# Kernel optimization log

Measured on AMD Instinct MI355X. Metric: run time of the kernel, lower is better.

The kernel has to match this reference:

```python
import jax, jax.numpy as jnp
import numpy as np

B, N, F, K = 64, 4096, 128, 64
N_STEP = 4
EPS_VAR = 1e-5


def setup_inputs() -> dict:
    key = jax.random.key(0)
    k1, k2, k3 = jax.random.split(key, 3)
    emb_in = jax.random.normal(k1, (B, N, F), dtype=jnp.float32)
    # number of valid nodes per sample; must be > K so init indices are valid
    batch_nb_nodes = jax.random.randint(k2, (B,), K + 1, N + 1).astype(jnp.int32)
    mask = (jnp.arange(N)[None, :] < batch_nb_nodes[:, None]).astype(jnp.float32)
    fc_w = jax.random.normal(k3, (1, F), dtype=jnp.float32) / np.float32(np.sqrt(F))
    fc_b = jnp.zeros((1,), dtype=jnp.float32)
    init_idx = jnp.arange(K, dtype=jnp.int32)  # replaces np.random.choice
    return {"emb_in": emb_in, "mask": mask, "fc_w": fc_w, "fc_b": fc_b,
            "batch_nb_nodes": batch_nb_nodes, "init_idx": init_idx}


def spatialnorm(emb, batch_nb_nodes, mask):
    # masked per-sample, per-feature standardization over the node axis
    n = batch_nb_nodes.astype(emb.dtype)[:, None, None]        # [B,1,1]
    m = mask[:, :, None]                                       # [B,N,1]
    mean = (emb * m).sum(axis=1, keepdims=True) / n            # [B,1,F]
    var = (((emb - mean) ** 2) * m).sum(axis=1, keepdims=True) / n
    x = (emb - mean) / jnp.sqrt(var + EPS_VAR) * m
    return x, mean, var


def expectation(x, mu):
    # squared L2 dists via expansion; avoids the [B,N,K,F] diff tensor
    x2 = (x * x).sum(-1)                                       # [B,N]
    m2 = (mu * mu).sum(-1)                                     # [B,K]
    xm = jnp.einsum('bnf,bkf->bnk', x, mu)                     # [B,N,K]
    norm = x2[:, :, None] - 2.0 * xm + m2[:, None, :]
    likelihood = jnp.exp(-0.5 * norm) + 1e-20
    P = likelihood / (likelihood.sum(axis=2, keepdims=True) + 1e-40)
    return P


def maximization(x, P):
    # mu = P^T X  (note: original does NOT divide by cluster mass)
    return jnp.einsum('bnk,bnf->bkf', P, x)


def reference(emb_in, mask, fc_w, fc_b, batch_nb_nodes, init_idx):
    x, _, _ = spatialnorm(emb_in, batch_nb_nodes, mask)
    mu = x[:, init_idx]                                        # [B,K,F]
    for _ in range(N_STEP):
        P = expectation(x, mu)
        mu = maximization(x, P)
    out = jnp.einsum('bkf,of->bko', mu, fc_w) + fc_b           # fc(mu): [B,K,1]
    out = out[..., 0].mean(axis=1)                             # [B]
    return jax.nn.sigmoid(out)
```

## Files before the change

### kernel.cpp

```cpp
#include <hip/hip_runtime.h>
#include <math.h>

#define BB 64
#define NN 4096
#define FF 128
#define KK 64
#define TILE 128
#define NSTEP 4
#define SPB 32

typedef short bf16x8 __attribute__((ext_vector_type(8)));
typedef float f32x4 __attribute__((ext_vector_type(4)));

__device__ __forceinline__ ushort f2bf(float f) {
    union { float f; unsigned u; } c; c.f = f;
    unsigned r = c.u + 0x7FFFu + ((c.u >> 16) & 1u);
    return (ushort)(r >> 16);
}
__device__ __forceinline__ float bf2f(ushort h) {
    union { unsigned u; float f; } c; c.u = ((unsigned)h) << 16;
    return c.f;
}

__global__ void k_stats_part(const float* __restrict__ emb, const int* __restrict__ nbv,
                             float* __restrict__ spart) {
    int b = blockIdx.y, s = blockIdx.x;
    int nb = nbv[b];
    int t = threadIdx.x;
    int c = t & 31, rr = t >> 5;
    int n0 = s * (NN / SPB);
    int n1 = min(n0 + NN / SPB, nb);
    float4 s1 = {0,0,0,0}, s2 = {0,0,0,0};
    const float4* base = (const float4*)(emb + (size_t)b * NN * FF);
    for (int n = n0 + rr; n < n1; n += 8) {
        float4 e = base[(size_t)n * 32 + c];
        s1.x += e.x; s1.y += e.y; s1.z += e.z; s1.w += e.w;
        s2.x += e.x*e.x; s2.y += e.y*e.y; s2.z += e.z*e.z; s2.w += e.w*e.w;
    }
    __shared__ __align__(16) float4 r1[8][32];
    __shared__ __align__(16) float4 r2[8][32];
    r1[rr][c] = s1; r2[rr][c] = s2;
    __syncthreads();
    if (t < 32) {
        float4 a1 = r1[0][t], a2 = r2[0][t];
        #pragma unroll
        for (int r = 1; r < 8; ++r) {
            float4 u = r1[r][t], v = r2[r][t];
            a1.x+=u.x; a1.y+=u.y; a1.z+=u.z; a1.w+=u.w;
            a2.x+=v.x; a2.y+=v.y; a2.z+=v.z; a2.w+=v.w;
        }
        ((float4*)(spart + ((size_t)(b*SPB+s)*2 + 0)*FF))[t] = a1;
        ((float4*)(spart + ((size_t)(b*SPB+s)*2 + 1)*FF))[t] = a2;
    }
}

__global__ void k_stats_fin(const float* __restrict__ spart, const int* __restrict__ nbv,
                            float* __restrict__ meanp, float* __restrict__ rstdp) {
    int b = blockIdx.x, f = threadIdx.x;
    float s1 = 0.f, s2 = 0.f;
    for (int s = 0; s < SPB; ++s) {
        s1 += spart[((size_t)(b*SPB+s)*2 + 0)*FF + f];
        s2 += spart[((size_t)(b*SPB+s)*2 + 1)*FF + f];
    }
    float nb = (float)nbv[b];
    float mean = s1 / nb;
    float var = s2 / nb - mean * mean;
    meanp[b*FF + f] = mean;
    rstdp[b*FF + f] = rsqrtf(var + 1e-5f);
}

__global__ void k_init(const float* __restrict__ emb, const int* __restrict__ nbv,
                       const int* __restrict__ init_idx,
                       const float* __restrict__ meanp, const float* __restrict__ rstdp,
                       float* __restrict__ mu) {
    size_t i = (size_t)blockIdx.x * 256 + threadIdx.x;
    int f = (int)(i & 127);
    int k = (int)((i >> 7) & 63);
    int b = (int)(i >> 13);
    int row = init_idx[k];
    float v = 0.f;
    if (row < nbv[b]) {
        float e = emb[((size_t)b * NN + row) * FF + f];
        v = (e - meanp[b*FF + f]) * rstdp[b*FF + f];
    }
    mu[i] = v;
}

__global__ void k_split(const float* __restrict__ mu, ushort* __restrict__ muh,
                        ushort* __restrict__ mul, float* __restrict__ m2g) {
    int b = blockIdx.x, t = threadIdx.x;
    int k = t >> 2, q = t & 3;
    size_t base = ((size_t)b * KK + k) * FF + q * 32;
    float m2 = 0.f;
    #pragma unroll
    for (int it = 0; it < 8; ++it) {
        float4 v = *(const float4*)(mu + base + it*4);
        m2 += v.x*v.x + v.y*v.y + v.z*v.z + v.w*v.w;
        ushort4 h4, l4;
        h4.x = f2bf(v.x); l4.x = f2bf(v.x - bf2f(h4.x));
        h4.y = f2bf(v.y); l4.y = f2bf(v.y - bf2f(h4.y));
        h4.z = f2bf(v.z); l4.z = f2bf(v.z - bf2f(h4.z));
        h4.w = f2bf(v.w); l4.w = f2bf(v.w - bf2f(h4.w));
        *(ushort4*)(muh + base + it*4) = h4;
        *(ushort4*)(mul + base + it*4) = l4;
    }
    m2 += __shfl_xor(m2, 1); m2 += __shfl_xor(m2, 2);
    if (q == 0) m2g[b*KK + k] = m2;
}

__global__ void k_zero(float* __restrict__ p) {
    size_t i = (size_t)blockIdx.x * 256 + threadIdx.x;
    ((float4*)p)[i] = make_float4(0.f, 0.f, 0.f, 0.f);
}

__global__ __launch_bounds__(1024, 4) void k_em3(const float* __restrict__ emb,
                                                 const int* __restrict__ nbv,
                                                 const float* __restrict__ meanp,
                                                 const float* __restrict__ rstdp,
                                                 const ushort* __restrict__ muh,
                                                 const ushort* __restrict__ mul,
                                                 const float* __restrict__ m2g,
                                                 float* __restrict__ mu_out) {
    __shared__ __align__(16) ushort xTh[FF * 64];
    __shared__ __align__(16) ushort xTl[FF * 64];
    __shared__ __align__(16) ushort pTh[KK * TILE];
    __shared__ __align__(16) ushort pTl[KK * TILE];

    int bb = blockIdx.y, tt = blockIdx.x;
    int nb = nbv[bb];
    int row0 = tt * TILE;
    if (row0 >= nb) return;
    int t = threadIdx.x;
    int lane = t & 63, w = t >> 6;
    int b = lane & 15, g = lane >> 4;

    const float* mnB = meanp + bb * FF;
    const float* rsB = rstdp + bb * FF;

    f32x4 acc1[4];
    float a2 = 0.f;

    if (w < 8) {
        #pragma unroll
        for (int kt = 0; kt < 4; ++kt) acc1[kt] = (f32x4){0.f,0.f,0.f,0.f};
        int nA = row0 + 16*w + b;
        const float* erow = emb + ((size_t)bb * NN + nA) * FF;
        const ushort* muhB = muh + (size_t)bb * KK * FF;
        const ushort* mulB = mul + (size_t)bb * KK * FF;
        #pragma unroll
        for (int kk = 0; kk < 4; ++kk) {
            int f0 = kk*32 + g*8;
            float4 e0 = *(const float4*)(erow + f0);
            float4 e1 = *(const float4*)(erow + f0 + 4);
            float4 m0 = *(const float4*)(mnB + f0);
            float4 m1 = *(const float4*)(mnB + f0 + 4);
            float4 r0 = *(const float4*)(rsB + f0);
            float4 r1 = *(const float4*)(rsB + f0 + 4);
            float vv[8];
            vv[0] = (e0.x - m0.x)*r0.x; vv[1] = (e0.y - m0.y)*r0.y;
            vv[2] = (e0.z - m0.z)*r0.z; vv[3] = (e0.w - m0.w)*r0.w;
            vv[4] = (e1.x - m1.x)*r1.x; vv[5] = (e1.y - m1.y)*r1.y;
            vv[6] = (e1.z - m1.z)*r1.z; vv[7] = (e1.w - m1.w)*r1.w;
            bf16x8 ah, al;
            #pragma unroll
            for (int i = 0; i < 8; ++i) {
                a2 += vv[i]*vv[i];
                ushort h = f2bf(vv[i]);
                ah[i] = (short)h;
                al[i] = (short)f2bf(vv[i] - bf2f(h));
            }
            #pragma unroll
            for (int kt = 0; kt < 4; ++kt) {
                size_t mo = (size_t)(kt*16 + b) * FF + f0;
                bf16x8 Bh = *(const bf16x8*)(muhB + mo);
                bf16x8 Bl = *(const bf16x8*)(mulB + mo);
                acc1[kt] = __builtin_amdgcn_mfma_f32_16x16x32_bf16(ah, Bh, acc1[kt], 0, 0, 0);
                acc1[kt] = __builtin_amdgcn_mfma_f32_16x16x32_bf16(ah, Bl, acc1[kt], 0, 0, 0);
                acc1[kt] = __builtin_amdgcn_mfma_f32_16x16x32_bf16(al, Bh, acc1[kt], 0, 0, 0);
            }
        }
        a2 += __shfl_xor(a2, 16);
        a2 += __shfl_xor(a2, 32);
    } else {
        int t2 = t - 512;
        int nl = t2 & 63;
        int fq = t2 >> 6;
        int gn = row0 + nl;
        bool valid = gn < nb;
        const float* er = emb + ((size_t)bb * NN + gn) * FF;
        #pragma unroll
        for (int it = 0; it < 4; ++it) {
            int f4 = fq + 8*it;
            float4 e = valid ? *(const float4*)(er + 4*f4) : make_float4(0.f,0.f,0.f,0.f);
            float4 mn = *(const float4*)(mnB + 4*f4);
            float4 rs = *(const float4*)(rsB + 4*f4);
            float vx[4];
            vx[0] = valid ? (e.x - mn.x)*rs.x : 0.f;
            vx[1] = valid ? (e.y - mn.y)*rs.y : 0.f;
            vx[2] = valid ? (e.z - mn.z)*rs.z : 0.f;
            vx[3] = valid ? (e.w - mn.w)*rs.w : 0.f;
            #pragma unroll
            for (int ei = 0; ei < 4; ++ei) {
                int f = 4*f4 + ei;
                ushort h = f2bf(vx[ei]);
                ushort l = f2bf(vx[ei] - bf2f(h));
                int idx = f*64 + ((((nl>>3) ^ (f&7)) << 3) | (nl & 7));
                xTh[idx] = h;
                xTl[idx] = l;
            }
        }
    }
    __syncthreads();

    if (w < 8) {
        float x2v[4], m2v[4];
        #pragma unroll
        for (int j = 0; j < 4; ++j) x2v[j] = __shfl(a2, 4*g + j);
        #pragma unroll
        for (int kt = 0; kt < 4; ++kt) m2v[kt] = m2g[bb*KK + kt*16 + b];
        float lik[4][4];
        float tot[4] = {0.f, 0.f, 0.f, 0.f};
        #pragma unroll
        for (int kt = 0; kt < 4; ++kt)
            #pragma unroll
            for (int j = 0; j < 4; ++j) {
                float s = acc1[kt][j];
                float L = expf(-0.5f * (x2v[j] - 2.f*s + m2v[kt])) + 1e-20f;
                lik[kt][j] = L;
                tot[j] += L;
            }
        #pragma unroll
        for (int j = 0; j < 4; ++j) {
            tot[j] += __shfl_xor(tot[j], 1);
            tot[j] += __shfl_xor(tot[j], 2);
            tot[j] += __shfl_xor(tot[j], 4);
            tot[j] += __shfl_xor(tot[j], 8);
            tot[j] = 1.f / (tot[j] + 1e-40f);
        }
        int np = 16*w + 4*g;
        #pragma unroll
        for (int kt = 0; kt < 4; ++kt) {
            int k = kt*16 + b;
            ushort4 uh, ul;
            float P0 = lik[kt][0]*tot[0]; uh.x = f2bf(P0); ul.x = f2bf(P0 - bf2f(uh.x));
            float P1 = lik[kt][1]*tot[1]; uh.y = f2bf(P1); ul.y = f2bf(P1 - bf2f(uh.y));
            float P2 = lik[kt][2]*tot[2]; uh.z = f2bf(P2); ul.z = f2bf(P2 - bf2f(uh.z));
            float P3 = lik[kt][3]*tot[3]; uh.w = f2bf(P3); ul.w = f2bf(P3 - bf2f(uh.w));
            int idx = k*TILE + (((np>>3) ^ (k&7)) << 3) + (np & 7);
            *(ushort4*)(&pTh[idx]) = uh;
            *(ushort4*)(&pTl[idx]) = ul;
        }
    }
    __syncthreads();

    int mt2 = w & 3;
    int fpair = w >> 2;
    f32x4 c0 = {0.f,0.f,0.f,0.f}, c1 = {0.f,0.f,0.f,0.f};
    int kA = 16*mt2 + b;
    int fB0 = 16*(2*fpair) + b;
    int fB1 = 16*(2*fpair + 1) + b;

    #pragma unroll
    for (int ns = 0; ns < 2; ++ns) {
        int gp = 4*ns + g;
        int gx = 4*ns + g;
        int ia = kA*TILE + ((gp ^ (kA&7)) << 3);
        bf16x8 Ah = *(const bf16x8*)(&pTh[ia]);
        bf16x8 Al = *(const bf16x8*)(&pTl[ia]);
        int ib0 = fB0*64 + ((gx ^ (fB0&7)) << 3);
        int ib1 = fB1*64 + ((gx ^ (fB1&7)) << 3);
        bf16x8 B0h = *(const bf16x8*)(&xTh[ib0]);
        bf16x8 B0l = *(const bf16x8*)(&xTl[ib0]);
        bf16x8 B1h = *(const bf16x8*)(&xTh[ib1]);
        bf16x8 B1l = *(const bf16x8*)(&xTl[ib1]);
        c0 = __builtin_amdgcn_mfma_f32_16x16x32_bf16(Ah, B0h, c0, 0, 0, 0);
        c0 = __builtin_amdgcn_mfma_f32_16x16x32_bf16(Ah, B0l, c0, 0, 0, 0);
        c0 = __builtin_amdgcn_mfma_f32_16x16x32_bf16(Al, B0h, c0, 0, 0, 0);
        c1 = __builtin_amdgcn_mfma_f32_16x16x32_bf16(Ah, B1h, c1, 0, 0, 0);
        c1 = __builtin_amdgcn_mfma_f32_16x16x32_bf16(Ah, B1l, c1, 0, 0, 0);
        c1 = __builtin_amdgcn_mfma_f32_16x16x32_bf16(Al, B1h, c1, 0, 0, 0);
    }
    __syncthreads();

    {
        int nl = t & 63;
        int fq = t >> 6;
        int gn = row0 + 64 + nl;
        bool valid = gn < nb;
        const float* er = emb + ((size_t)bb * NN + gn) * FF;
        #pragma unroll
        for (int it = 0; it < 2; ++it) {
            int f4 = fq + 16*it;
            float4 e = valid ? *(const float4*)(er + 4*f4) : make_float4(0.f,0.f,0.f,0.f);
            float4 mn = *(const float4*)(mnB + 4*f4);
            float4 rs = *(const float4*)(rsB + 4*f4);
            float vx[4];
            vx[0] = valid ? (e.x - mn.x)*rs.x : 0.f;
            vx[1] = valid ? (e.y - mn.y)*rs.y : 0.f;
            vx[2] = valid ? (e.z - mn.z)*rs.z : 0.f;
            vx[3] = valid ? (e.w - mn.w)*rs.w : 0.f;
            #pragma unroll
            for (int ei = 0; ei < 4; ++ei) {
                int f = 4*f4 + ei;
                ushort h = f2bf(vx[ei]);
                ushort l = f2bf(vx[ei] - bf2f(h));
                int idx = f*64 + ((((nl>>3) ^ (f&7)) << 3) | (nl & 7));
                xTh[idx] = h;
                xTl[idx] = l;
            }
        }
    }
    __syncthreads();

    #pragma unroll
    for (int ns = 2; ns < 4; ++ns) {
        int gp = 4*ns + g;
        int gx = 4*(ns - 2) + g;
        int ia = kA*TILE + ((gp ^ (kA&7)) << 3);
        bf16x8 Ah = *(const bf16x8*)(&pTh[ia]);
        bf16x8 Al = *(const bf16x8*)(&pTl[ia]);
        int ib0 = fB0*64 + ((gx ^ (fB0&7)) << 3);
        int ib1 = fB1*64 + ((gx ^ (fB1&7)) << 3);
        bf16x8 B0h = *(const bf16x8*)(&xTh[ib0]);
        bf16x8 B0l = *(const bf16x8*)(&xTl[ib0]);
        bf16x8 B1h = *(const bf16x8*)(&xTh[ib1]);
        bf16x8 B1l = *(const bf16x8*)(&xTl[ib1]);
        c0 = __builtin_amdgcn_mfma_f32_16x16x32_bf16(Ah, B0h, c0, 0, 0, 0);
        c0 = __builtin_amdgcn_mfma_f32_16x16x32_bf16(Ah, B0l, c0, 0, 0, 0);
        c0 = __builtin_amdgcn_mfma_f32_16x16x32_bf16(Al, B0h, c0, 0, 0, 0);
        c1 = __builtin_amdgcn_mfma_f32_16x16x32_bf16(Ah, B1h, c1, 0, 0, 0);
        c1 = __builtin_amdgcn_mfma_f32_16x16x32_bf16(Ah, B1l, c1, 0, 0, 0);
        c1 = __builtin_amdgcn_mfma_f32_16x16x32_bf16(Al, B1h, c1, 0, 0, 0);
    }

    {
        float* mo = mu_out + (size_t)bb * KK * FF;
        #pragma unroll
        for (int j = 0; j < 4; ++j) {
            int ko = 16*mt2 + 4*g + j;
            unsafeAtomicAdd(mo + (size_t)ko * FF + fB0, c0[j]);
            unsafeAtomicAdd(mo + (size_t)ko * FF + fB1, c1[j]);
        }
    }
}

__global__ void k_final(const float* __restrict__ mu, const float* __restrict__ fc_w,
                        const float* __restrict__ fc_b, float* __restrict__ out) {
    int b = blockIdx.x, t = threadIdx.x;
    int k = t >> 2, q = t & 3;
    const float* m = mu + ((size_t)b * KK + k) * FF + q * 32;
    const float* wv = fc_w + q * 32;
    float s = 0.f;
    #pragma unroll
    for (int i = 0; i < 32; ++i) s = fmaf(m[i], wv[i], s);
    s += __shfl_xor(s, 1); s += __shfl_xor(s, 2);
    __shared__ float kd[KK];
    if (q == 0) kd[k] = s;
    __syncthreads();
    if (t < 64) {
        float v = kd[t];
        v += __shfl_xor(v, 1);  v += __shfl_xor(v, 2);  v += __shfl_xor(v, 4);
        v += __shfl_xor(v, 8);  v += __shfl_xor(v, 16); v += __shfl_xor(v, 32);
        if (t == 0) {
            float o = v / (float)KK + fc_b[0];
            out[b] = 1.f / (1.f + expf(-o));
        }
    }
}

extern "C" void kernel_launch(void* const* d_in, const int* in_sizes, int n_in,
                              void* d_out, int out_size, void* d_ws, size_t ws_size,
                              hipStream_t stream) {
    const float* emb      = (const float*)d_in[0];
    const float* fc_w     = (const float*)d_in[2];
    const float* fc_b     = (const float*)d_in[3];
    const int*   nbv      = (const int*)d_in[4];
    const int*   init_idx = (const int*)d_in[5];
    float* out = (float*)d_out;

    float* wsf   = (float*)d_ws;
    float* meanp = wsf;
    float* rstdp = meanp + BB*FF;
    float* spart = rstdp + BB*FF;
    float* muA   = spart + (size_t)BB*SPB*2*FF;
    float* muB   = muA + (size_t)BB*KK*FF;
    float* m2g   = muB + (size_t)BB*KK*FF;
    ushort* muh  = (ushort*)(m2g + BB*KK);
    ushort* mul  = muh + (size_t)BB*KK*FF;

    k_stats_part<<<dim3(SPB, BB), 256, 0, stream>>>(emb, nbv, spart);
    k_stats_fin<<<BB, 128, 0, stream>>>(spart, nbv, meanp, rstdp);
    k_init<<<(BB*KK*FF)/256, 256, 0, stream>>>(emb, nbv, init_idx, meanp, rstdp, muA);

    const int zblocks = (BB*KK*FF/4) / 256;
    for (int step = 0; step < NSTEP; ++step) {
        const float* mu_in = (step & 1) ? muB : muA;
        float* mu_out      = (step & 1) ? muA : muB;
        k_split<<<BB, 256, 0, stream>>>(mu_in, muh, mul, m2g);
        k_zero<<<zblocks, 256, 0, stream>>>(mu_out);
        k_em3<<<dim3(NN/TILE, BB), 1024, 0, stream>>>(emb, nbv, meanp, rstdp,
                                                      muh, mul, m2g, mu_out);
    }
    k_final<<<BB, 256, 0, stream>>>(muA, fc_w, fc_b, out);
}
```

Before: 778.7 us.

## Loop each EM block over several node tiles and replace atomics with partial-sum reduction

```diff
diff --git a/kernel.cpp b/kernel.cpp
--- a/kernel.cpp
+++ b/kernel.cpp
@@ -8,6 +8,7 @@
 #define TILE 128
 #define NSTEP 4
 #define SPB 32
+#define NTB 8
 
 typedef short bf16x8 __attribute__((ext_vector_type(8)));
 typedef float f32x4 __attribute__((ext_vector_type(4)));
@@ -108,28 +109,21 @@
     if (q == 0) m2g[b*KK + k] = m2;
 }
 
-__global__ void k_zero(float* __restrict__ p) {
-    size_t i = (size_t)blockIdx.x * 256 + threadIdx.x;
-    ((float4*)p)[i] = make_float4(0.f, 0.f, 0.f, 0.f);
-}
-
-__global__ __launch_bounds__(1024, 4) void k_em3(const float* __restrict__ emb,
+__global__ __launch_bounds__(1024, 8) void k_em4(const float* __restrict__ emb,
                                                  const int* __restrict__ nbv,
                                                  const float* __restrict__ meanp,
                                                  const float* __restrict__ rstdp,
                                                  const ushort* __restrict__ muh,
                                                  const ushort* __restrict__ mul,
                                                  const float* __restrict__ m2g,
-                                                 float* __restrict__ mu_out) {
+                                                 float* __restrict__ partial) {
     __shared__ __align__(16) ushort xTh[FF * 64];
     __shared__ __align__(16) ushort xTl[FF * 64];
     __shared__ __align__(16) ushort pTh[KK * TILE];
     __shared__ __align__(16) ushort pTl[KK * TILE];
 
-    int bb = blockIdx.y, tt = blockIdx.x;
+    int bb = blockIdx.y, t0 = blockIdx.x;
     int nb = nbv[bb];
-    int row0 = tt * TILE;
-    if (row0 >= nb) return;
     int t = threadIdx.x;
     int lane = t & 63, w = t >> 6;
     int b = lane & 15, g = lane >> 4;
@@ -137,210 +131,247 @@
     const float* mnB = meanp + bb * FF;
     const float* rsB = rstdp + bb * FF;
 
-    f32x4 acc1[4];
-    float a2 = 0.f;
-
-    if (w < 8) {
-        #pragma unroll
-        for (int kt = 0; kt < 4; ++kt) acc1[kt] = (f32x4){0.f,0.f,0.f,0.f};
-        int nA = row0 + 16*w + b;
-        const float* erow = emb + ((size_t)bb * NN + nA) * FF;
-        const ushort* muhB = muh + (size_t)bb * KK * FF;
-        const ushort* mulB = mul + (size_t)bb * KK * FF;
-        #pragma unroll
-        for (int kk = 0; kk < 4; ++kk) {
-            int f0 = kk*32 + g*8;
-            float4 e0 = *(const float4*)(erow + f0);
-            float4 e1 = *(const float4*)(erow + f0 + 4);
-            float4 m0 = *(const float4*)(mnB + f0);
-            float4 m1 = *(const float4*)(mnB + f0 + 4);
-            float4 r0 = *(const float4*)(rsB + f0);
-            float4 r1 = *(const float4*)(rsB + f0 + 4);
-            float vv[8];
-            vv[0] = (e0.x - m0.x)*r0.x; vv[1] = (e0.y - m0.y)*r0.y;
-            vv[2] = (e0.z - m0.z)*r0.z; vv[3] = (e0.w - m0.w)*r0.w;
-            vv[4] = (e1.x - m1.x)*r1.x; vv[5] = (e1.y - m1.y)*r1.y;
-            vv[6] = (e1.z - m1.z)*r1.z; vv[7] = (e1.w - m1.w)*r1.w;
-            bf16x8 ah, al;
-            #pragma unroll
-            for (int i = 0; i < 8; ++i) {
-                a2 += vv[i]*vv[i];
-                ushort h = f2bf(vv[i]);
-                ah[i] = (short)h;
-                al[i] = (short)f2bf(vv[i] - bf2f(h));
-            }
-            #pragma unroll
-            for (int kt = 0; kt < 4; ++kt) {
-                size_t mo = (size_t)(kt*16 + b) * FF + f0;
-                bf16x8 Bh = *(const bf16x8*)(muhB + mo);
-                bf16x8 Bl = *(const bf16x8*)(mulB + mo);
-                acc1[kt] = __builtin_amdgcn_mfma_f32_16x16x32_bf16(ah, Bh, acc1[kt], 0, 0, 0);
-                acc1[kt] = __builtin_amdgcn_mfma_f32_16x16x32_bf16(ah, Bl, acc1[kt], 0, 0, 0);
-                acc1[kt] = __builtin_amdgcn_mfma_f32_16x16x32_bf16(al, Bh, acc1[kt], 0, 0, 0);
-            }
-        }
-        a2 += __shfl_xor(a2, 16);
-        a2 += __shfl_xor(a2, 32);
-    } else {
-        int t2 = t - 512;
-        int nl = t2 & 63;
-        int fq = t2 >> 6;
-        int gn = row0 + nl;
-        bool valid = gn < nb;
-        const float* er = emb + ((size_t)bb * NN + gn) * FF;
-        #pragma unroll
-        for (int it = 0; it < 4; ++it) {
-            int f4 = fq + 8*it;
-            float4 e = valid ? *(const float4*)(er + 4*f4) : make_float4(0.f,0.f,0.f,0.f);
-            float4 mn = *(const float4*)(mnB + 4*f4);
-            float4 rs = *(const float4*)(rsB + 4*f4);
-            float vx[4];
-            vx[0] = valid ? (e.x - mn.x)*rs.x : 0.f;
-            vx[1] = valid ? (e.y - mn.y)*rs.y : 0.f;
-            vx[2] = valid ? (e.z - mn.z)*rs.z : 0.f;
-            vx[3] = valid ? (e.w - mn.w)*rs.w : 0.f;
-            #pragma unroll
-            for (int ei = 0; ei < 4; ++ei) {
-                int f = 4*f4 + ei;
-                ushort h = f2bf(vx[ei]);
-                ushort l = f2bf(vx[ei] - bf2f(h));
-                int idx = f*64 + ((((nl>>3) ^ (f&7)) << 3) | (nl & 7));
-                xTh[idx] = h;
-                xTl[idx] = l;
-            }
-        }
-    }
-    __syncthreads();
-
-    if (w < 8) {
-        float x2v[4], m2v[4];
-        #pragma unroll
-        for (int j = 0; j < 4; ++j) x2v[j] = __shfl(a2, 4*g + j);
-        #pragma unroll
-        for (int kt = 0; kt < 4; ++kt) m2v[kt] = m2g[bb*KK + kt*16 + b];
-        float lik[4][4];
-        float tot[4] = {0.f, 0.f, 0.f, 0.f};
-        #pragma unroll
-        for (int kt = 0; kt < 4; ++kt)
-            #pragma unroll
-            for (int j = 0; j < 4; ++j) {
-                float s = acc1[kt][j];
-                float L = expf(-0.5f * (x2v[j] - 2.f*s + m2v[kt])) + 1e-20f;
-                lik[kt][j] = L;
-                tot[j] += L;
-            }
-        #pragma unroll
-        for (int j = 0; j < 4; ++j) {
-            tot[j] += __shfl_xor(tot[j], 1);
-            tot[j] += __shfl_xor(tot[j], 2);
-            tot[j] += __shfl_xor(tot[j], 4);
-            tot[j] += __shfl_xor(tot[j], 8);
-            tot[j] = 1.f / (tot[j] + 1e-40f);
-        }
-        int np = 16*w + 4*g;
-        #pragma unroll
-        for (int kt = 0; kt < 4; ++kt) {
-            int k = kt*16 + b;
-            ushort4 uh, ul;
-            float P0 = lik[kt][0]*tot[0]; uh.x = f2bf(P0); ul.x = f2bf(P0 - bf2f(uh.x));
-            float P1 = lik[kt][1]*tot[1]; uh.y = f2bf(P1); ul.y = f2bf(P1 - bf2f(uh.y));
-            float P2 = lik[kt][2]*tot[2]; uh.z = f2bf(P2); ul.z = f2bf(P2 - bf2f(uh.z));
-            float P3 = lik[kt][3]*tot[3]; uh.w = f2bf(P3); ul.w = f2bf(P3 - bf2f(uh.w));
-            int idx = k*TILE + (((np>>3) ^ (k&7)) << 3) + (np & 7);
-            *(ushort4*)(&pTh[idx]) = uh;
-            *(ushort4*)(&pTl[idx]) = ul;
-        }
-    }
-    __syncthreads();
-
     int mt2 = w & 3;
     int fpair = w >> 2;
-    f32x4 c0 = {0.f,0.f,0.f,0.f}, c1 = {0.f,0.f,0.f,0.f};
     int kA = 16*mt2 + b;
     int fB0 = 16*(2*fpair) + b;
     int fB1 = 16*(2*fpair + 1) + b;
-
-    #pragma unroll
-    for (int ns = 0; ns < 2; ++ns) {
-        int gp = 4*ns + g;
-        int gx = 4*ns + g;
-        int ia = kA*TILE + ((gp ^ (kA&7)) << 3);
-        bf16x8 Ah = *(const bf16x8*)(&pTh[ia]);
-        bf16x8 Al = *(const bf16x8*)(&pTl[ia]);
-        int ib0 = fB0*64 + ((gx ^ (fB0&7)) << 3);
-        int ib1 = fB1*64 + ((gx ^ (fB1&7)) << 3);
-        bf16x8 B0h = *(const bf16x8*)(&xTh[ib0]);
-        bf16x8 B0l = *(const bf16x8*)(&xTl[ib0]);
-        bf16x8 B1h = *(const bf16x8*)(&xTh[ib1]);
-        bf16x8 B1l = *(const bf16x8*)(&xTl[ib1]);
-        c0 = __builtin_amdgcn_mfma_f32_16x16x32_bf16(Ah, B0h, c0, 0, 0, 0);
-        c0 = __builtin_amdgcn_mfma_f32_16x16x32_bf16(Ah, B0l, c0, 0, 0, 0);
-        c0 = __builtin_amdgcn_mfma_f32_16x16x32_bf16(Al, B0h, c0, 0, 0, 0);
-        c1 = __builtin_amdgcn_mfma_f32_16x16x32_bf16(Ah, B1h, c1, 0, 0, 0);
-        c1 = __builtin_amdgcn_mfma_f32_16x16x32_bf16(Ah, B1l, c1, 0, 0, 0);
-        c1 = __builtin_amdgcn_mfma_f32_16x16x32_bf16(Al, B1h, c1, 0, 0, 0);
-    }
-    __syncthreads();
+    f32x4 c0 = {0.f,0.f,0.f,0.f}, c1 = {0.f,0.f,0.f,0.f};
+
+    #pragma unroll 1
+    for (int it = 0; it < 4; ++it) {
+        int tt = t0 + NTB * it;
+        int row0 = tt * TILE;
+        if (row0 >= nb) break;
+
+        f32x4 acc1[4];
+        float a2 = 0.f;
+
+        if (w < 8) {
+            #pragma unroll
+            for (int kt = 0; kt < 4; ++kt) acc1[kt] = (f32x4){0.f,0.f,0.f,0.f};
+            int nA = row0 + 16*w + b;
+            const float* erow = emb + ((size_t)bb * NN + nA) * FF;
+            const ushort* muhB = muh + (size_t)bb * KK * FF;
+            const ushort* mulB = mul + (size_t)bb * KK * FF;
+            #pragma unroll
+            for (int kk = 0; kk < 4; ++kk) {
+                int f0 = kk*32 + g*8;
+                float4 e0 = *(const float4*)(erow + f0);
+                float4 e1 = *(const float4*)(erow + f0 + 4);
+                float4 m0 = *(const float4*)(mnB + f0);
+                float4 m1 = *(const float4*)(mnB + f0 + 4);
+                float4 r0 = *(const float4*)(rsB + f0);
+                float4 r1 = *(const float4*)(rsB + f0 + 4);
+                float vv[8];
+                vv[0] = (e0.x - m0.x)*r0.x; vv[1] = (e0.y - m0.y)*r0.y;
+                vv[2] = (e0.z - m0.z)*r0.z; vv[3] = (e0.w - m0.w)*r0.w;
+                vv[4] = (e1.x - m1.x)*r1.x; vv[5] = (e1.y - m1.y)*r1.y;
+                vv[6] = (e1.z - m1.z)*r1.z; vv[7] = (e1.w - m1.w)*r1.w;
+                bf16x8 ah, al;
+                #pragma unroll
+                for (int i = 0; i < 8; ++i) {
+                    a2 += vv[i]*vv[i];
+                    ushort h = f2bf(vv[i]);
+                    ah[i] = (short)h;
+                    al[i] = (short)f2bf(vv[i] - bf2f(h));
+                }
+                #pragma unroll
+                for (int kt = 0; kt < 4; ++kt) {
+                    size_t mo = (size_t)(kt*16 + b) * FF + f0;
+                    bf16x8 Bh = *(const bf16x8*)(muhB + mo);
+                    bf16x8 Bl = *(const bf16x8*)(mulB + mo);
+                    acc1[kt] = __builtin_amdgcn_mfma_f32_16x16x32_bf16(ah, Bh, acc1[kt], 0, 0, 0);
+                    acc1[kt] = __builtin_amdgcn_mfma_f32_16x16x32_bf16(ah, Bl, acc1[kt], 0, 0, 0);
+                    acc1[kt] = __builtin_amdgcn_mfma_f32_16x16x32_bf16(al, Bh, acc1[kt], 0, 0, 0);
+                }
+            }
+            a2 += __shfl_xor(a2, 16);
+            a2 += __shfl_xor(a2, 32);
+        } else {
+            int t2 = t - 512;
+            int nl = t2 & 63;
+            int fq = t2 >> 6;
+            int gn = row0 + nl;
+            bool valid = gn < nb;
+            const float* er = emb + ((size_t)bb * NN + gn) * FF;
+            #pragma unroll
+            for (int itr = 0; itr < 4; ++itr) {
+                int f4 = fq + 8*itr;
+                float4 e = valid ? *(const float4*)(er + 4*f4) : make_float4(0.f,0.f,0.f,0.f);
+                float4 mn = *(const float4*)(mnB + 4*f4);
+                float4 rs = *(const float4*)(rsB + 4*f4);
+                float vx[4];
+                vx[0] = valid ? (e.x - mn.x)*rs.x : 0.f;
+                vx[1] = valid ? (e.y - mn.y)*rs.y : 0.f;
+                vx[2] = valid ? (e.z - mn.z)*rs.z : 0.f;
+                vx[3] = valid ? (e.w - mn.w)*rs.w : 0.f;
+                #pragma unroll
+                for (int ei = 0; ei < 4; ++ei) {
+                    int f = 4*f4 + ei;
+                    ushort h = f2bf(vx[ei]);
+                    ushort l = f2bf(vx[ei] - bf2f(h));
+                    int idx = f*64 + ((((nl>>3) ^ (f&7)) << 3) | (nl & 7));
+                    xTh[idx] = h;
+                    xTl[idx] = l;
+                }
+            }
+        }
+        __syncthreads();
+
+        if (w < 8) {
+            float x2v[4], m2v[4];
+            #pragma unroll
+            for (int j = 0; j < 4; ++j) x2v[j] = __shfl(a2, 4*g + j);
+            #pragma unroll
+            for (int kt = 0; kt < 4; ++kt) m2v[kt] = m2g[bb*KK + kt*16 + b];
+            float lik[4][4];
+            float tot[4] = {0.f, 0.f, 0.f, 0.f};
+            #pragma unroll
+            for (int kt = 0; kt < 4; ++kt)
+                #pragma unroll
+                for (int j = 0; j < 4; ++j) {
+                    float s = acc1[kt][j];
+                    float L = expf(-0.5f * (x2v[j] - 2.f*s + m2v[kt])) + 1e-20f;
+                    lik[kt][j] = L;
+                    tot[j] += L;
+                }
+            #pragma unroll
+            for (int j = 0; j < 4; ++j) {
+                tot[j] += __shfl_xor(tot[j], 1);
+                tot[j] += __shfl_xor(tot[j], 2);
+                tot[j] += __shfl_xor(tot[j], 4);
+                tot[j] += __shfl_xor(tot[j], 8);
+                tot[j] = 1.f / (tot[j] + 1e-40f);
+            }
+            int np = 16*w + 4*g;
+            #pragma unroll
+            for (int kt = 0; kt < 4; ++kt) {
+                int k = kt*16 + b;
+                ushort4 uh, ul;
+                float P0 = lik[kt][0]*tot[0]; uh.x = f2bf(P0); ul.x = f2bf(P0 - bf2f(uh.x));
+                float P1 = lik[kt][1]*tot[1]; uh.y = f2bf(P1); ul.y = f2bf(P1 - bf2f(uh.y));
+                float P2 = lik[kt][2]*tot[2]; uh.z = f2bf(P2); ul.z = f2bf(P2 - bf2f(uh.z));
+                float P3 = lik[kt][3]*tot[3]; uh.w = f2bf(P3); ul.w = f2bf(P3 - bf2f(uh.w));
+                int idx = k*TILE + (((np>>3) ^ (k&7)) << 3) + (np & 7);
+                *(ushort4*)(&pTh[idx]) = uh;
+                *(ushort4*)(&pTl[idx]) = ul;
+            }
+        }
+        __syncthreads();
+
+        #pragma unroll
+        for (int ns = 0; ns < 2; ++ns) {
+            int gp = 4*ns + g;
+            int gx = 4*ns + g;
+            int ia = kA*TILE + ((gp ^ (kA&7)) << 3);
+            bf16x8 Ah = *(const bf16x8*)(&pTh[ia]);
+            bf16x8 Al = *(const bf16x8*)(&pTl[ia]);
+            int ib0 = fB0*64 + ((gx ^ (fB0&7)) << 3);
+            int ib1 = fB1*64 + ((gx ^ (fB1&7)) << 3);
+            bf16x8 B0h = *(const bf16x8*)(&xTh[ib0]);
+            bf16x8 B0l = *(const bf16x8*)(&xTl[ib0]);
+            bf16x8 B1h = *(const bf16x8*)(&xTh[ib1]);
+            bf16x8 B1l = *(const bf16x8*)(&xTl[ib1]);
+            c0 = __builtin_amdgcn_mfma_f32_16x16x32_bf16(Ah, B0h, c0, 0, 0, 0);
+            c0 = __builtin_amdgcn_mfma_f32_16x16x32_bf16(Ah, B0l, c0, 0, 0, 0);
+            c0 = __builtin_amdgcn_mfma_f32_16x16x32_bf16(Al, B0h, c0, 0, 0, 0);
+            c1 = __builtin_amdgcn_mfma_f32_16x16x32_bf16(Ah, B1h, c1, 0, 0, 0);
+            c1 = __builtin_amdgcn_mfma_f32_16x16x32_bf16(Ah, B1l, c1, 0, 0, 0);
+            c1 = __builtin_amdgcn_mfma_f32_16x16x32_bf16(Al, B1h, c1, 0, 0, 0);
+        }
+        __syncthreads();
+
+        {
+            int nl = t & 63;
+            int fq = t >> 6;
+            int gn = row0 + 64 + nl;
+            bool valid = gn < nb;
+            const float* er = emb + ((size_t)bb * NN + gn) * FF;
+            #pragma unroll
+            for (int itr = 0; itr < 2; ++itr) {
+                int f4 = fq + 16*itr;
+                float4 e = valid ? *(const float4*)(er + 4*f4) : make_float4(0.f,0.f,0.f,0.f);
+                float4 mn = *(const float4*)(mnB + 4*f4);
+                float4 rs = *(const float4*)(rsB + 4*f4);
+                float vx[4];
+                vx[0] = valid ? (e.x - mn.x)*rs.x : 0.f;
+                vx[1] = valid ? (e.y - mn.y)*rs.y : 0.f;
+                vx[2] = valid ? (e.z - mn.z)*rs.z : 0.f;
+                vx[3] = valid ? (e.w - mn.w)*rs.w : 0.f;
+                #pragma unroll
+                for (int ei = 0; ei < 4; ++ei) {
+                    int f = 4*f4 + ei;
+                    ushort h = f2bf(vx[ei]);
+                    ushort l = f2bf(vx[ei] - bf2f(h));
+                    int idx = f*64 + ((((nl>>3) ^ (f&7)) << 3) | (nl & 7));
+                    xTh[idx] = h;
+                    xTl[idx] = l;
+                }
+            }
+        }
+        __syncthreads();
+
+        #pragma unroll
+        for (int ns = 2; ns < 4; ++ns) {
+            int gp = 4*ns + g;
+            int gx = 4*(ns - 2) + g;
+            int ia = kA*TILE + ((gp ^ (kA&7)) << 3);
+            bf16x8 Ah = *(const bf16x8*)(&pTh[ia]);
+            bf16x8 Al = *(const bf16x8*)(&pTl[ia]);
+            int ib0 = fB0*64 + ((gx ^ (fB0&7)) << 3);
+            int ib1 = fB1*64 + ((gx ^ (fB1&7)) << 3);
+            bf16x8 B0h = *(const bf16x8*)(&xTh[ib0]);
+            bf16x8 B0l = *(const bf16x8*)(&xTl[ib0]);
+            bf16x8 B1h = *(const bf16x8*)(&xTh[ib1]);
+            bf16x8 B1l = *(const bf16x8*)(&xTl[ib1]);
+            c0 = __builtin_amdgcn_mfma_f32_16x16x32_bf16(Ah, B0h, c0, 0, 0, 0);
+            c0 = __builtin_amdgcn_mfma_f32_16x16x32_bf16(Ah, B0l, c0, 0, 0, 0);
+            c0 = __builtin_amdgcn_mfma_f32_16x16x32_bf16(Al, B0h, c0, 0, 0, 0);
+            c1 = __builtin_amdgcn_mfma_f32_16x16x32_bf16(Ah, B1h, c1, 0, 0, 0);
+            c1 = __builtin_amdgcn_mfma_f32_16x16x32_bf16(Ah, B1l, c1, 0, 0, 0);
+            c1 = __builtin_amdgcn_mfma_f32_16x16x32_bf16(Al, B1h, c1, 0, 0, 0);
+        }
+        __syncthreads();
+    }
 
     {
-        int nl = t & 63;
-        int fq = t >> 6;
-        int gn = row0 + 64 + nl;
-        bool valid = gn < nb;
-        const float* er = emb + ((size_t)bb * NN + gn) * FF;
-        #pragma unroll
-        for (int it = 0; it < 2; ++it) {
-            int f4 = fq + 16*it;
-            float4 e = valid ? *(const float4*)(er + 4*f4) : make_float4(0.f,0.f,0.f,0.f);
-            float4 mn = *(const float4*)(mnB + 4*f4);
-            float4 rs = *(const float4*)(rsB + 4*f4);
-            float vx[4];
-            vx[0] = valid ? (e.x - mn.x)*rs.x : 0.f;
-            vx[1] = valid ? (e.y - mn.y)*rs.y : 0.f;
-            vx[2] = valid ? (e.z - mn.z)*rs.z : 0.f;
-            vx[3] = valid ? (e.w - mn.w)*rs.w : 0.f;
-            #pragma unroll
-            for (int ei = 0; ei < 4; ++ei) {
-                int f = 4*f4 + ei;
-                ushort h = f2bf(vx[ei]);
-                ushort l = f2bf(vx[ei] - bf2f(h));
-                int idx = f*64 + ((((nl>>3) ^ (f&7)) << 3) | (nl & 7));
-                xTh[idx] = h;
-                xTl[idx] = l;
-            }
-        }
-    }
-    __syncthreads();
-
-    #pragma unroll
-    for (int ns = 2; ns < 4; ++ns) {
-        int gp = 4*ns + g;
-        int gx = 4*(ns - 2) + g;
-        int ia = kA*TILE + ((gp ^ (kA&7)) << 3);
-        bf16x8 Ah = *(const bf16x8*)(&pTh[ia]);
-        bf16x8 Al = *(const bf16x8*)(&pTl[ia]);
-        int ib0 = fB0*64 + ((gx ^ (fB0&7)) << 3);
-        int ib1 = fB1*64 + ((gx ^ (fB1&7)) << 3);
-        bf16x8 B0h = *(const bf16x8*)(&xTh[ib0]);
-        bf16x8 B0l = *(const bf16x8*)(&xTl[ib0]);
-        bf16x8 B1h = *(const bf16x8*)(&xTh[ib1]);
-        bf16x8 B1l = *(const bf16x8*)(&xTl[ib1]);
-        c0 = __builtin_amdgcn_mfma_f32_16x16x32_bf16(Ah, B0h, c0, 0, 0, 0);
-        c0 = __builtin_amdgcn_mfma_f32_16x16x32_bf16(Ah, B0l, c0, 0, 0, 0);
-        c0 = __builtin_amdgcn_mfma_f32_16x16x32_bf16(Al, B0h, c0, 0, 0, 0);
-        c1 = __builtin_amdgcn_mfma_f32_16x16x32_bf16(Ah, B1h, c1, 0, 0, 0);
-        c1 = __builtin_amdgcn_mfma_f32_16x16x32_bf16(Ah, B1l, c1, 0, 0, 0);
-        c1 = __builtin_amdgcn_mfma_f32_16x16x32_bf16(Al, B1h, c1, 0, 0, 0);
-    }
-
-    {
-        float* mo = mu_out + (size_t)bb * KK * FF;
+        float* pp = partial + ((size_t)t0 * BB + bb) * KK * FF;
         #pragma unroll
         for (int j = 0; j < 4; ++j) {
             int ko = 16*mt2 + 4*g + j;
-            unsafeAtomicAdd(mo + (size_t)ko * FF + fB0, c0[j]);
-            unsafeAtomicAdd(mo + (size_t)ko * FF + fB1, c1[j]);
-        }
+            pp[(size_t)ko * FF + fB0] = c0[j];
+            pp[(size_t)ko * FF + fB1] = c1[j];
+        }
+    }
+}
+
+__global__ void k_reduce8(const float* __restrict__ partial, float* __restrict__ muF,
+                          ushort* __restrict__ muh, ushort* __restrict__ mul,
+                          float* __restrict__ m2g) {
+    int b = blockIdx.x;
+    int t = threadIdx.x;
+    int w = t >> 6, lane = t & 63;
+    #pragma unroll
+    for (int i = 0; i < 8; ++i) {
+        int k = w * 8 + i;
+        size_t off = ((size_t)b * KK + k) * FF + lane * 2;
+        float sx = 0.f, sy = 0.f;
+        #pragma unroll
+        for (int sl = 0; sl < NTB; ++sl) {
+            float2 v = *(const float2*)(partial + (size_t)sl * BB * KK * FF + off);
+            sx += v.x; sy += v.y;
+        }
+        *(float2*)(muF + off) = make_float2(sx, sy);
+        ushort2 h2, l2;
+        h2.x = f2bf(sx); l2.x = f2bf(sx - bf2f(h2.x));
+        h2.y = f2bf(sy); l2.y = f2bf(sy - bf2f(h2.y));
+        *(ushort2*)(muh + off) = h2;
+        *(ushort2*)(mul + off) = l2;
+        float q = sx*sx + sy*sy;
+        q += __shfl_xor(q, 1); q += __shfl_xor(q, 2); q += __shfl_xor(q, 4);
+        q += __shfl_xor(q, 8); q += __shfl_xor(q, 16); q += __shfl_xor(q, 32);
+        if (lane == 0) m2g[b * KK + k] = q;
     }
 }
 
@@ -382,24 +413,21 @@
     float* meanp = wsf;
     float* rstdp = meanp + BB*FF;
     float* spart = rstdp + BB*FF;
-    float* muA   = spart + (size_t)BB*SPB*2*FF;
-    float* muB   = muA + (size_t)BB*KK*FF;
-    float* m2g   = muB + (size_t)BB*KK*FF;
+    float* muF   = spart + (size_t)BB*SPB*2*FF;
+    float* m2g   = muF + (size_t)BB*KK*FF;
     ushort* muh  = (ushort*)(m2g + BB*KK);
     ushort* mul  = muh + (size_t)BB*KK*FF;
+    float* part  = (float*)(mul + (size_t)BB*KK*FF);
 
     k_stats_part<<<dim3(SPB, BB), 256, 0, stream>>>(emb, nbv, spart);
     k_stats_fin<<<BB, 128, 0, stream>>>(spart, nbv, meanp, rstdp);
-    k_init<<<(BB*KK*FF)/256, 256, 0, stream>>>(emb, nbv, init_idx, meanp, rstdp, muA);
-
-    const int zblocks = (BB*KK*FF/4) / 256;
+    k_init<<<(BB*KK*FF)/256, 256, 0, stream>>>(emb, nbv, init_idx, meanp, rstdp, muF);
+    k_split<<<BB, 256, 0, stream>>>(muF, muh, mul, m2g);
+
     for (int step = 0; step < NSTEP; ++step) {
-        const float* mu_in = (step & 1) ? muB : muA;
-        float* mu_out      = (step & 1) ? muA : muB;
-        k_split<<<BB, 256, 0, stream>>>(mu_in, muh, mul, m2g);
-        k_zero<<<zblocks, 256, 0, stream>>>(mu_out);
-        k_em3<<<dim3(NN/TILE, BB), 1024, 0, stream>>>(emb, nbv, meanp, rstdp,
-                                                      muh, mul, m2g, mu_out);
-    }
-    k_final<<<BB, 256, 0, stream>>>(muA, fc_w, fc_b, out);
-}
+        k_em4<<<dim3(NTB, BB), 1024, 0, stream>>>(emb, nbv, meanp, rstdp,
+                                                  muh, mul, m2g, part);
+        k_reduce8<<<BB, 512, 0, stream>>>(part, muF, muh, mul, m2g);
+    }
+    k_final<<<BB, 256, 0, stream>>>(muF, fc_w, fc_b, out);
+}
```

Measured after the change: 1.564 ms. 2.01x slower.
